# Performance work log

Hardware: AMD Instinct MI355X
Metric: run time of the kernel (lower is better)

The kernel has to match this reference:

```python
import jax, jax.numpy as jnp
import numpy as np


def gcn_conv(x, edge_index, W, b):
    # PyG GCNConv: h = x @ W; add self-loops; symmetric D^-1/2 (A+I) D^-1/2 aggregation; + bias
    n = x.shape[0]
    h = x @ W  # [N, out]
    loop = jnp.arange(n, dtype=edge_index.dtype)
    src = jnp.concatenate([edge_index[0], loop])  # message sources
    dst = jnp.concatenate([edge_index[1], loop])  # message targets
    ones = jnp.ones(dst.shape[0], dtype=h.dtype)
    deg = jax.ops.segment_sum(ones, dst, num_segments=n)  # in-degree incl. self-loop
    dinv = jnp.where(deg > 0, jax.lax.rsqrt(deg), 0.0)
    norm = dinv[src] * dinv[dst]  # [E+N]
    msg = h[src] * norm[:, None]  # gather + scale
    out = jax.ops.segment_sum(msg, dst, num_segments=n)  # scatter-add
    return out + b


def setup_inputs() -> dict:
    key = jax.random.key(0)
    ks = jax.random.split(key, 6)
    N, E, D = 100000, 600000, 128
    x = jax.random.normal(ks[0], (N, D), dtype=jnp.float32)
    edge_index = jax.random.randint(ks[1], (2, E), 0, N, dtype=jnp.int64)
    s = 1.0 / np.sqrt(D)
    W1 = jax.random.normal(ks[2], (D, D), dtype=jnp.float32) * s
    b1 = jnp.zeros((D,), dtype=jnp.float32)
    W2 = jax.random.normal(ks[3], (2 * D, D), dtype=jnp.float32) * (1.0 / np.sqrt(2 * D))
    b2 = jnp.zeros((D,), dtype=jnp.float32)
    Wout = jax.random.normal(ks[4], (D, 1), dtype=jnp.float32) * s
    bout = jnp.zeros((1,), dtype=jnp.float32)
    return {"x": x, "edge_index": edge_index, "W1": W1, "b1": b1,
            "W2": W2, "b2": b2, "Wout": Wout, "bout": bout}


def reference(x, edge_index, W1, b1, W2, b2, Wout, bout):
    y = gcn_conv(x, edge_index, W1, b1)          # [N, D]
    y = jnp.concatenate([x, y], axis=-1)          # [N, 2D]
    y = jax.nn.leaky_relu(y, negative_slope=0.01)
    z = gcn_conv(y, edge_index, W2, b2)           # [N, D]
    z = jax.nn.leaky_relu(z, negative_slope=0.01)
    return z @ Wout + bout                        # [N, 1]
```

## Files before the change

kernel.cpp:

```cpp
#include <hip/hip_runtime.h>

#define DIM 128
#define CAP 48

typedef _Float16 half8 __attribute__((ext_vector_type(8)));
typedef float f32x4 __attribute__((ext_vector_type(4)));

__device__ __forceinline__ float lrelu(float v) { return v > 0.f ? v : 0.01f * v; }

__device__ __forceinline__ void gather_sum(
    const _Float16* __restrict__ H, const int* __restrict__ sl,
    int cnt, int g, int zr, float a[8]) {
    int c16 = cnt < 16 ? cnt : 16;
    int sidb = (g < c16) ? sl[g] : zr;
    half8 v[8];
#pragma unroll
    for (int j = 0; j < 8; ++j) {
        int s = __shfl(sidb, j, 16);
        v[j] = *(const half8*)&H[(size_t)s * DIM + g * 8];
    }
#pragma unroll
    for (int j = 0; j < 8; ++j)
#pragma unroll
        for (int e = 0; e < 8; ++e) a[e] += (float)v[j][e];
    if (cnt > 8) {
#pragma unroll
        for (int j = 0; j < 8; ++j) {
            int s = __shfl(sidb, 8 + j, 16);
            v[j] = *(const half8*)&H[(size_t)s * DIM + g * 8];
        }
#pragma unroll
        for (int j = 0; j < 8; ++j)
#pragma unroll
            for (int e = 0; e < 8; ++e) a[e] += (float)v[j][e];
        if (cnt > 16) {
            for (int base = 16; base < cnt; base += 16) {
                int m = cnt - base;
                if (m > 16) m = 16;
                int sb = (g < m) ? sl[base + g] : zr;
                for (int j = 0; j < m; ++j) {
                    int s = __shfl(sb, j, 16);
                    half8 vv = *(const half8*)&H[(size_t)s * DIM + g * 8];
#pragma unroll
                    for (int e = 0; e < 8; ++e) a[e] += (float)vv[e];
                }
            }
        }
    }
}

__device__ __forceinline__ void gather_sum_scaled(
    const _Float16* __restrict__ H, const int* __restrict__ cursor,
    const int* __restrict__ sl, int cnt, int g, int zr, float a[8]) {
    int c16 = cnt < 16 ? cnt : 16;
    int sidb = (g < c16) ? sl[g] : zr;
    float dvb = rsqrtf((float)cursor[sidb] + 1.0f);
    half8 v[8];
#pragma unroll
    for (int j = 0; j < 8; ++j) {
        int s = __shfl(sidb, j, 16);
        v[j] = *(const half8*)&H[(size_t)s * DIM + g * 8];
    }
#pragma unroll
    for (int j = 0; j < 8; ++j) {
        float sc = __shfl(dvb, j, 16);
#pragma unroll
        for (int e = 0; e < 8; ++e) a[e] = fmaf((float)v[j][e], sc, a[e]);
    }
    if (cnt > 8) {
#pragma unroll
        for (int j = 0; j < 8; ++j) {
            int s = __shfl(sidb, 8 + j, 16);
            v[j] = *(const half8*)&H[(size_t)s * DIM + g * 8];
        }
#pragma unroll
        for (int j = 0; j < 8; ++j) {
            float sc = __shfl(dvb, 8 + j, 16);
#pragma unroll
            for (int e = 0; e < 8; ++e) a[e] = fmaf((float)v[j][e], sc, a[e]);
        }
        if (cnt > 16) {
            for (int base = 16; base < cnt; base += 16) {
                int m = cnt - base;
                if (m > 16) m = 16;
                int sb = (g < m) ? sl[base + g] : zr;
                float db2 = rsqrtf((float)cursor[sb] + 1.0f);
                for (int j = 0; j < m; ++j) {
                    int s = __shfl(sb, j, 16);
                    float sc = __shfl(db2, j, 16);
                    half8 vv = *(const half8*)&H[(size_t)s * DIM + g * 8];
#pragma unroll
                    for (int e = 0; e < 8; ++e) a[e] = fmaf((float)vv[e], sc, a[e]);
                }
            }
        }
    }
}

__global__ __launch_bounds__(256) void k_init(
    int* __restrict__ cursor, int na4, int nzb,
    const float* __restrict__ W1, _Float16* __restrict__ Wp1,
    const float* __restrict__ W2, _Float16* __restrict__ Wp2,
    _Float16* __restrict__ zrow, _Float16* __restrict__ zrow2) {
    int b = blockIdx.x;
    if (b < nzb) {
        int i = b * 256 + threadIdx.x;
        if (i < na4) {
            int4 z = make_int4(0, 0, 0, 0);
            *(int4*)&cursor[i * 4] = z;
        }
        return;
    }
    b -= nzb;
    if (b >= 192) {
        if (threadIdx.x < 16) {
            half8 z = 0;
            *(half8*)&zrow[threadIdx.x * 8] = z;
            *(half8*)&zrow2[threadIdx.x * 8] = z;
        }
        return;
    }
    const float* W;
    _Float16* Wp;
    int tid2;
    if (b < 64) { W = W1; Wp = Wp1; tid2 = b * 256 + threadIdx.x; }
    else        { W = W2; Wp = Wp2; tid2 = (b - 64) * 256 + threadIdx.x; }
    int jj = tid2 & 7;
    int frag = tid2 >> 3;
    int l = frag & 63;
    int cb = (frag >> 6) & 7;
    int kb = frag >> 9;
    Wp[tid2] = (_Float16)W[(size_t)(kb * 32 + ((l >> 4) << 3) + jj) * DIM + cb * 16 + (l & 15)];
}

__global__ __launch_bounds__(256, 2) void k_front(
    const float* __restrict__ x, const _Float16* __restrict__ Wp1,
    _Float16* __restrict__ hs, int n, int gb,
    const int* __restrict__ esrc, const int* __restrict__ edst,
    int* __restrict__ cursor, int* __restrict__ srcs, int E) {
    __shared__ _Float16 Hs[64 * 136];
    const int bb = blockIdx.x;
    if (bb >= gb) {
        int i = (bb - gb) * 256 + threadIdx.x;
        if (i < E) {
            int d = edst[i];
            int p = atomicAdd(&cursor[d], 1);
            if (p < CAP) srcs[(size_t)d * CAP + p] = esrc[i];
        }
        return;
    }
    const int tid = threadIdx.x;
    const int w = tid >> 6, l = tid & 63;
    const int row0 = bb * 64;
    const int arow = row0 + w * 16 + (l & 15);
    const int kq = (l >> 4) << 3;
    const bool ok = arow < n;
    const float* xr = &x[(size_t)arow * DIM + kq];

    f32x4 ah[8];
#pragma unroll
    for (int cb = 0; cb < 8; ++cb) {
        f32x4 z = {0.f, 0.f, 0.f, 0.f};
        ah[cb] = z;
    }

#pragma unroll
    for (int kb = 0; kb < 4; ++kb) {
        float4 v0 = make_float4(0.f, 0.f, 0.f, 0.f), v1 = v0;
        if (ok) {
            v0 = *(const float4*)&xr[kb * 32];
            v1 = *(const float4*)&xr[kb * 32 + 4];
        }
        half8 a;
        a[0] = (_Float16)v0.x; a[1] = (_Float16)v0.y;
        a[2] = (_Float16)v0.z; a[3] = (_Float16)v0.w;
        a[4] = (_Float16)v1.x; a[5] = (_Float16)v1.y;
        a[6] = (_Float16)v1.z; a[7] = (_Float16)v1.w;
#pragma unroll
        for (int cb = 0; cb < 8; ++cb) {
            half8 bf = *(const half8*)&Wp1[((kb * 8 + cb) * 64 + l) * 8];
            ah[cb] = __builtin_amdgcn_mfma_f32_16x16x32_f16(a, bf, ah[cb], 0, 0, 0);
        }
    }
    const int orow = w * 16 + ((l >> 4) << 2);
    const int oc = l & 15;
#pragma unroll
    for (int reg = 0; reg < 4; ++reg) {
#pragma unroll
        for (int cb = 0; cb < 8; ++cb)
            Hs[(orow + reg) * 136 + cb * 16 + oc] = (_Float16)ah[cb][reg];
    }
    __syncthreads();
#pragma unroll
    for (int it = 0; it < 4; ++it) {
        int i = it * 256 + tid;
        int r = i >> 4, c = (i & 15) * 8;
        if (row0 + r < n)
            *(half8*)&hs[(size_t)(row0 + r) * DIM + c] = *(const half8*)&Hs[r * 136 + c];
    }
}

__global__ __launch_bounds__(256, 2) void k_mm2g(
    const float* __restrict__ x, const _Float16* __restrict__ hs,
    const int* __restrict__ cursor, const int* __restrict__ srcs,
    const float* __restrict__ b1, const _Float16* __restrict__ Wp2,
    _Float16* __restrict__ hs2, int n) {
    __shared__ _Float16 LS[64 * 136];
    const int tid = threadIdx.x;
    const int w = tid >> 6, l = tid & 63;
    const int g = tid & 15, gid = tid >> 4;
    const int row0 = blockIdx.x * 64;

    f32x4 acc[8];
#pragma unroll
    for (int cb = 0; cb < 8; ++cb) {
        f32x4 z = {0.f, 0.f, 0.f, 0.f};
        acc[cb] = z;
    }

#pragma unroll
    for (int it = 0; it < 4; ++it) {
        int node = row0 + it * 16 + gid;
        half8 o = 0;
        if (node < n) {
            int rawc = cursor[node];
            int cnt = rawc > CAP ? CAP : rawc;
            const int* sl = &srcs[(size_t)node * CAP];
            float d = rsqrtf((float)rawc + 1.0f);
            half8 h = *(const half8*)&hs[(size_t)node * DIM + g * 8];
            float a[8];
#pragma unroll
            for (int e = 0; e < 8; ++e) a[e] = (float)h[e] * d;
            gather_sum_scaled(hs, cursor, sl, cnt, g, n, a);
            const float4 bb0 = *(const float4*)&b1[g * 8];
            const float4 bb1 = *(const float4*)&b1[g * 8 + 4];
            o[0] = (_Float16)lrelu(fmaf(a[0], d, bb0.x));
            o[1] = (_Float16)lrelu(fmaf(a[1], d, bb0.y));
            o[2] = (_Float16)lrelu(fmaf(a[2], d, bb0.z));
            o[3] = (_Float16)lrelu(fmaf(a[3], d, bb0.w));
            o[4] = (_Float16)lrelu(fmaf(a[4], d, bb1.x));
            o[5] = (_Float16)lrelu(fmaf(a[5], d, bb1.y));
            o[6] = (_Float16)lrelu(fmaf(a[6], d, bb1.z));
            o[7] = (_Float16)lrelu(fmaf(a[7], d, bb1.w));
        }
        *(half8*)&LS[(((it * 4 + (g >> 2)) * 64) + (g & 3) * 16 + gid) * 8] = o;
    }

    {
        const int arow = row0 + w * 16 + (l & 15);
        const int kq = (l >> 4) << 3;
        const bool ok = arow < n;
        const float* xr = &x[(size_t)arow * DIM + kq];
#pragma unroll
        for (int kb = 0; kb < 4; ++kb) {
            float4 v0 = make_float4(0.f, 0.f, 0.f, 0.f), v1 = v0;
            if (ok) {
                v0 = *(const float4*)&xr[kb * 32];
                v1 = *(const float4*)&xr[kb * 32 + 4];
            }
            half8 a, al;
            a[0] = (_Float16)v0.x; a[1] = (_Float16)v0.y;
            a[2] = (_Float16)v0.z; a[3] = (_Float16)v0.w;
            a[4] = (_Float16)v1.x; a[5] = (_Float16)v1.y;
            a[6] = (_Float16)v1.z; a[7] = (_Float16)v1.w;
#pragma unroll
            for (int e = 0; e < 8; ++e) {
                _Float16 t = a[e];
                al[e] = (t > (_Float16)0.f) ? t : t * (_Float16)0.01f;
            }
#pragma unroll
            for (int cb = 0; cb < 8; ++cb) {
                half8 bf = *(const half8*)&Wp2[((kb * 8 + cb) * 64 + l) * 8];
                acc[cb] = __builtin_amdgcn_mfma_f32_16x16x32_f16(al, bf, acc[cb], 0, 0, 0);
            }
        }
    }
    __syncthreads();

#pragma unroll
    for (int kb = 0; kb < 4; ++kb) {
        half8 a = *(const half8*)&LS[((w * 4 + kb) * 64 + l) * 8];
#pragma unroll
        for (int cb = 0; cb < 8; ++cb) {
            half8 bf = *(const half8*)&Wp2[(((kb + 4) * 8 + cb) * 64 + l) * 8];
            acc[cb] = __builtin_amdgcn_mfma_f32_16x16x32_f16(a, bf, acc[cb], 0, 0, 0);
        }
    }
    __syncthreads();
    const int orow = w * 16 + ((l >> 4) << 2);
    const int oc = l & 15;
#pragma unroll
    for (int reg = 0; reg < 4; ++reg) {
        int grow = row0 + orow + reg;
        float d = (grow < n) ? rsqrtf((float)cursor[grow] + 1.0f) : 0.f;
#pragma unroll
        for (int cb = 0; cb < 8; ++cb)
            LS[(orow + reg) * 136 + cb * 16 + oc] = (_Float16)(acc[cb][reg] * d);
    }
    __syncthreads();
#pragma unroll
    for (int it = 0; it < 4; ++it) {
        int i = it * 256 + tid;
        int r = i >> 4, c = (i & 15) * 8;
        if (row0 + r < n)
            *(half8*)&hs2[(size_t)(row0 + r) * DIM + c] = *(const half8*)&LS[r * 136 + c];
    }
}

__global__ __launch_bounds__(256) void k_gather2(
    const _Float16* __restrict__ hs2, const int* __restrict__ cursor,
    const int* __restrict__ srcs, const float* __restrict__ b2,
    const float* __restrict__ wout, const float* __restrict__ bout,
    float* __restrict__ out, int n) {
    const int node = blockIdx.x * 16 + (threadIdx.x >> 4);
    const int g = threadIdx.x & 15;
    if (node >= n) return;
    int rawc = cursor[node];
    int cnt = rawc > CAP ? CAP : rawc;
    const int* sl = &srcs[(size_t)node * CAP];
    half8 h = *(const half8*)&hs2[(size_t)node * DIM + g * 8];
    float a[8];
#pragma unroll
    for (int e = 0; e < 8; ++e) a[e] = (float)h[e];
    gather_sum(hs2, sl, cnt, g, n, a);
    float d = rsqrtf((float)rawc + 1.0f);
    const float4 bb0 = *(const float4*)&b2[g * 8];
    const float4 bb1 = *(const float4*)&b2[g * 8 + 4];
    const float4 wv0 = *(const float4*)&wout[g * 8];
    const float4 wv1 = *(const float4*)&wout[g * 8 + 4];
    float s = lrelu(fmaf(a[0], d, bb0.x)) * wv0.x + lrelu(fmaf(a[1], d, bb0.y)) * wv0.y +
              lrelu(fmaf(a[2], d, bb0.z)) * wv0.z + lrelu(fmaf(a[3], d, bb0.w)) * wv0.w +
              lrelu(fmaf(a[4], d, bb1.x)) * wv1.x + lrelu(fmaf(a[5], d, bb1.y)) * wv1.y +
              lrelu(fmaf(a[6], d, bb1.z)) * wv1.z + lrelu(fmaf(a[7], d, bb1.w)) * wv1.w;
#pragma unroll
    for (int off = 8; off > 0; off >>= 1) s += __shfl_down(s, off, 16);
    if (g == 0) out[node] = s + bout[0];
}

extern "C" void kernel_launch(void* const* d_in, const int* in_sizes, int n_in,
                              void* d_out, int out_size, void* d_ws, size_t ws_size,
                              hipStream_t stream) {
    const float* x    = (const float*)d_in[0];
    const int*   ei   = (const int*)d_in[1];
    const float* W1   = (const float*)d_in[2];
    const float* b1   = (const float*)d_in[3];
    const float* W2   = (const float*)d_in[4];
    const float* b2   = (const float*)d_in[5];
    const float* Wout = (const float*)d_in[6];
    const float* bout = (const float*)d_in[7];
    float* out = (float*)d_out;

    const int N = in_sizes[0] / DIM;
    const int E = in_sizes[1] / 2;
    const int* src = ei;
    const int* dst = ei + E;

    const int gb = (N + 63) / 64;
    const long long nx = (long long)N * DIM;

    size_t Na = ((size_t)N + 63) & ~(size_t)63;
    int* cursor   = (int*)d_ws;
    int* srcs     = cursor + Na;
    _Float16* Wp1 = (_Float16*)(srcs + (size_t)N * CAP);
    _Float16* Wp2 = Wp1 + 128 * 128;
    _Float16* hsb = Wp2 + 256 * 128;
    _Float16* hs2 = hsb + nx + DIM;

    const int eb = (E + 255) / 256;
    const int na4 = (int)(Na / 4);
    const int nzb = (na4 + 255) / 256;

    k_init<<<nzb + 193, 256, 0, stream>>>(cursor, na4, nzb, W1, Wp1, W2, Wp2,
                                          hsb + nx, hs2 + nx);
    k_front<<<gb + eb, 256, 0, stream>>>(x, Wp1, hsb, N, gb, src, dst, cursor, srcs, E);
    k_mm2g<<<gb, 256, 0, stream>>>(x, hsb, cursor, srcs, b1, Wp2, hs2, N);
    k_gather2<<<(N + 15) / 16, 256, 0, stream>>>(hs2, cursor, srcs, b2, Wout, bout, out, N);
}
```

Measured before the change: 213.2 us.

## Software-pipeline neighbor gathers with x-part MFMAs in layer-2 kernel

The mm2g kernel now hoists all per-node metadata loads (degree, first source ids, self row, x row) up front. It then interleaves the first 8-neighbor gather burst of each of the four node groups with the MFMAs for the x half of the concatenated input, using double-buffered half8 registers. This is meant to hide gather latency behind matrix work and to issue more memory requests in parallel. In exchange it raises register pressure at occupancy 2, and it extends the srcs workspace by one row so out-of-range nodes can be clamped to index n.

```diff
diff --git a/kernel.cpp b/kernel.cpp
--- a/kernel.cpp
+++ b/kernel.cpp
@@ -43,54 +43,6 @@
                     half8 vv = *(const half8*)&H[(size_t)s * DIM + g * 8];
 #pragma unroll
                     for (int e = 0; e < 8; ++e) a[e] += (float)vv[e];
-                }
-            }
-        }
-    }
-}
-
-__device__ __forceinline__ void gather_sum_scaled(
-    const _Float16* __restrict__ H, const int* __restrict__ cursor,
-    const int* __restrict__ sl, int cnt, int g, int zr, float a[8]) {
-    int c16 = cnt < 16 ? cnt : 16;
-    int sidb = (g < c16) ? sl[g] : zr;
-    float dvb = rsqrtf((float)cursor[sidb] + 1.0f);
-    half8 v[8];
-#pragma unroll
-    for (int j = 0; j < 8; ++j) {
-        int s = __shfl(sidb, j, 16);
-        v[j] = *(const half8*)&H[(size_t)s * DIM + g * 8];
-    }
-#pragma unroll
-    for (int j = 0; j < 8; ++j) {
-        float sc = __shfl(dvb, j, 16);
-#pragma unroll
-        for (int e = 0; e < 8; ++e) a[e] = fmaf((float)v[j][e], sc, a[e]);
-    }
-    if (cnt > 8) {
-#pragma unroll
-        for (int j = 0; j < 8; ++j) {
-            int s = __shfl(sidb, 8 + j, 16);
-            v[j] = *(const half8*)&H[(size_t)s * DIM + g * 8];
-        }
-#pragma unroll
-        for (int j = 0; j < 8; ++j) {
-            float sc = __shfl(dvb, 8 + j, 16);
-#pragma unroll
-            for (int e = 0; e < 8; ++e) a[e] = fmaf((float)v[j][e], sc, a[e]);
-        }
-        if (cnt > 16) {
-            for (int base = 16; base < cnt; base += 16) {
-                int m = cnt - base;
-                if (m > 16) m = 16;
-                int sb = (g < m) ? sl[base + g] : zr;
-                float db2 = rsqrtf((float)cursor[sb] + 1.0f);
-                for (int j = 0; j < m; ++j) {
-                    int s = __shfl(sb, j, 16);
-                    float sc = __shfl(db2, j, 16);
-                    half8 vv = *(const half8*)&H[(size_t)s * DIM + g * 8];
-#pragma unroll
-                    for (int e = 0; e < 8; ++e) a[e] = fmaf((float)vv[e], sc, a[e]);
                 }
             }
         }
@@ -211,6 +163,59 @@
     const int g = tid & 15, gid = tid >> 4;
     const int row0 = blockIdx.x * 64;
 
+    int nd[4]; bool nok[4]; int rawc[4]; int slraw[4]; half8 hself[4];
+#pragma unroll
+    for (int it = 0; it < 4; ++it) {
+        int node = row0 + it * 16 + gid;
+        nok[it] = node < n;
+        nd[it] = nok[it] ? node : n;
+        rawc[it] = cursor[nd[it]];
+        slraw[it] = srcs[(size_t)nd[it] * CAP + g];
+        hself[it] = *(const half8*)&hs[(size_t)nd[it] * DIM + g * 8];
+    }
+
+    const int arow = row0 + w * 16 + (l & 15);
+    const int kq = (l >> 4) << 3;
+    const bool ok = arow < n;
+    const float* xr = &x[(size_t)arow * DIM + kq];
+    float4 xv0[4], xv1[4];
+#pragma unroll
+    for (int kb = 0; kb < 4; ++kb) {
+        xv0[kb] = make_float4(0.f, 0.f, 0.f, 0.f);
+        xv1[kb] = xv0[kb];
+        if (ok) {
+            xv0[kb] = *(const float4*)&xr[kb * 32];
+            xv1[kb] = *(const float4*)&xr[kb * 32 + 4];
+        }
+    }
+    const float4 bb0 = *(const float4*)&b1[g * 8];
+    const float4 bb1 = *(const float4*)&b1[g * 8 + 4];
+
+    int cnt[4]; int sidb[4]; float dvbr[4];
+#pragma unroll
+    for (int it = 0; it < 4; ++it) {
+        int c = rawc[it] > CAP ? CAP : rawc[it];
+        cnt[it] = c;
+        int c16 = c < 16 ? c : 16;
+        sidb[it] = (g < c16) ? slraw[it] : n;
+        dvbr[it] = (float)cursor[sidb[it]];
+    }
+
+    half8 al[4];
+#pragma unroll
+    for (int kb = 0; kb < 4; ++kb) {
+        half8 a;
+        a[0] = (_Float16)xv0[kb].x; a[1] = (_Float16)xv0[kb].y;
+        a[2] = (_Float16)xv0[kb].z; a[3] = (_Float16)xv0[kb].w;
+        a[4] = (_Float16)xv1[kb].x; a[5] = (_Float16)xv1[kb].y;
+        a[6] = (_Float16)xv1[kb].z; a[7] = (_Float16)xv1[kb].w;
+#pragma unroll
+        for (int e = 0; e < 8; ++e) {
+            _Float16 t = a[e];
+            al[kb][e] = (t > (_Float16)0.f) ? t : t * (_Float16)0.01f;
+        }
+    }
+
     f32x4 acc[8];
 #pragma unroll
     for (int cb = 0; cb < 8; ++cb) {
@@ -218,63 +223,92 @@
         acc[cb] = z;
     }
 
-#pragma unroll
-    for (int it = 0; it < 4; ++it) {
-        int node = row0 + it * 16 + gid;
-        half8 o = 0;
-        if (node < n) {
-            int rawc = cursor[node];
-            int cnt = rawc > CAP ? CAP : rawc;
-            const int* sl = &srcs[(size_t)node * CAP];
-            float d = rsqrtf((float)rawc + 1.0f);
-            half8 h = *(const half8*)&hs[(size_t)node * DIM + g * 8];
-            float a[8];
-#pragma unroll
-            for (int e = 0; e < 8; ++e) a[e] = (float)h[e] * d;
-            gather_sum_scaled(hs, cursor, sl, cnt, g, n, a);
-            const float4 bb0 = *(const float4*)&b1[g * 8];
-            const float4 bb1 = *(const float4*)&b1[g * 8 + 4];
-            o[0] = (_Float16)lrelu(fmaf(a[0], d, bb0.x));
-            o[1] = (_Float16)lrelu(fmaf(a[1], d, bb0.y));
-            o[2] = (_Float16)lrelu(fmaf(a[2], d, bb0.z));
-            o[3] = (_Float16)lrelu(fmaf(a[3], d, bb0.w));
-            o[4] = (_Float16)lrelu(fmaf(a[4], d, bb1.x));
-            o[5] = (_Float16)lrelu(fmaf(a[5], d, bb1.y));
-            o[6] = (_Float16)lrelu(fmaf(a[6], d, bb1.z));
-            o[7] = (_Float16)lrelu(fmaf(a[7], d, bb1.w));
-        }
+#define ISSUE_BURST(buf, it)                                              \
+    do {                                                                  \
+        _Pragma("unroll") for (int j = 0; j < 8; ++j) {                   \
+            int s = __shfl(sidb[it], j, 16);                              \
+            buf[j] = *(const half8*)&hs[(size_t)s * DIM + g * 8];         \
+        }                                                                 \
+    } while (0)
+
+#define XMFMA(kb)                                                               \
+    do {                                                                        \
+        _Pragma("unroll") for (int cb = 0; cb < 8; ++cb) {                      \
+            half8 bf = *(const half8*)&Wp2[(((kb) * 8 + cb) * 64 + l) * 8];     \
+            acc[cb] = __builtin_amdgcn_mfma_f32_16x16x32_f16(al[kb], bf,        \
+                                                             acc[cb], 0, 0, 0); \
+        }                                                                       \
+    } while (0)
+
+    auto consume = [&](int it, half8* vb) {
+        float dself = rsqrtf((float)rawc[it] + 1.0f);
+        float dv = rsqrtf(dvbr[it] + 1.0f);
+        float a[8];
+#pragma unroll
+        for (int e = 0; e < 8; ++e) a[e] = (float)hself[it][e] * dself;
+#pragma unroll
+        for (int j = 0; j < 8; ++j) {
+            float sc = __shfl(dv, j, 16);
+#pragma unroll
+            for (int e = 0; e < 8; ++e) a[e] = fmaf((float)vb[j][e], sc, a[e]);
+        }
+        if (cnt[it] > 8) {
+#pragma unroll
+            for (int j = 0; j < 8; ++j) {
+                int s = __shfl(sidb[it], 8 + j, 16);
+                vb[j] = *(const half8*)&hs[(size_t)s * DIM + g * 8];
+            }
+#pragma unroll
+            for (int j = 0; j < 8; ++j) {
+                float sc = __shfl(dv, 8 + j, 16);
+#pragma unroll
+                for (int e = 0; e < 8; ++e) a[e] = fmaf((float)vb[j][e], sc, a[e]);
+            }
+            if (cnt[it] > 16) {
+                const int* sl = &srcs[(size_t)nd[it] * CAP];
+                for (int base = 16; base < cnt[it]; base += 16) {
+                    int m = cnt[it] - base;
+                    if (m > 16) m = 16;
+                    int sb = (g < m) ? sl[base + g] : n;
+                    float db2 = rsqrtf((float)cursor[sb] + 1.0f);
+                    for (int j = 0; j < m; ++j) {
+                        int s = __shfl(sb, j, 16);
+                        float sc = __shfl(db2, j, 16);
+                        half8 vv = *(const half8*)&hs[(size_t)s * DIM + g * 8];
+#pragma unroll
+                        for (int e = 0; e < 8; ++e) a[e] = fmaf((float)vv[e], sc, a[e]);
+                    }
+                }
+            }
+        }
+        half8 o;
+        o[0] = (_Float16)lrelu(fmaf(a[0], dself, bb0.x));
+        o[1] = (_Float16)lrelu(fmaf(a[1], dself, bb0.y));
+        o[2] = (_Float16)lrelu(fmaf(a[2], dself, bb0.z));
+        o[3] = (_Float16)lrelu(fmaf(a[3], dself, bb0.w));
+        o[4] = (_Float16)lrelu(fmaf(a[4], dself, bb1.x));
+        o[5] = (_Float16)lrelu(fmaf(a[5], dself, bb1.y));
+        o[6] = (_Float16)lrelu(fmaf(a[6], dself, bb1.z));
+        o[7] = (_Float16)lrelu(fmaf(a[7], dself, bb1.w));
+        if (!nok[it]) { half8 z = 0; o = z; }
         *(half8*)&LS[(((it * 4 + (g >> 2)) * 64) + (g & 3) * 16 + gid) * 8] = o;
-    }
-
-    {
-        const int arow = row0 + w * 16 + (l & 15);
-        const int kq = (l >> 4) << 3;
-        const bool ok = arow < n;
-        const float* xr = &x[(size_t)arow * DIM + kq];
-#pragma unroll
-        for (int kb = 0; kb < 4; ++kb) {
-            float4 v0 = make_float4(0.f, 0.f, 0.f, 0.f), v1 = v0;
-            if (ok) {
-                v0 = *(const float4*)&xr[kb * 32];
-                v1 = *(const float4*)&xr[kb * 32 + 4];
-            }
-            half8 a, al;
-            a[0] = (_Float16)v0.x; a[1] = (_Float16)v0.y;
-            a[2] = (_Float16)v0.z; a[3] = (_Float16)v0.w;
-            a[4] = (_Float16)v1.x; a[5] = (_Float16)v1.y;
-            a[6] = (_Float16)v1.z; a[7] = (_Float16)v1.w;
-#pragma unroll
-            for (int e = 0; e < 8; ++e) {
-                _Float16 t = a[e];
-                al[e] = (t > (_Float16)0.f) ? t : t * (_Float16)0.01f;
-            }
-#pragma unroll
-            for (int cb = 0; cb < 8; ++cb) {
-                half8 bf = *(const half8*)&Wp2[((kb * 8 + cb) * 64 + l) * 8];
-                acc[cb] = __builtin_amdgcn_mfma_f32_16x16x32_f16(al, bf, acc[cb], 0, 0, 0);
-            }
-        }
-    }
+    };
+
+    half8 vA[8], vB[8];
+    ISSUE_BURST(vA, 0);
+    XMFMA(0);
+    ISSUE_BURST(vB, 1);
+    XMFMA(1);
+    consume(0, vA);
+    ISSUE_BURST(vA, 2);
+    XMFMA(2);
+    consume(1, vB);
+    ISSUE_BURST(vB, 3);
+    XMFMA(3);
+    consume(2, vA);
+    consume(3, vB);
+#undef ISSUE_BURST
+#undef XMFMA
     __syncthreads();
 
 #pragma unroll
@@ -361,7 +395,7 @@
     size_t Na = ((size_t)N + 63) & ~(size_t)63;
     int* cursor   = (int*)d_ws;
     int* srcs     = cursor + Na;
-    _Float16* Wp1 = (_Float16*)(srcs + (size_t)N * CAP);
+    _Float16* Wp1 = (_Float16*)(srcs + ((size_t)N + 1) * CAP);
     _Float16* Wp2 = Wp1 + 128 * 128;
     _Float16* hsb = Wp2 + 256 * 128;
     _Float16* hs2 = hsb + nx + DIM;
```

Result: slower. 231.0 us (+8.4%).
